# Kernel tuning notes

Hardware: AMD Instinct MI355X
Metric: run time of the kernel (lower is better)

## Reference

```python
import jax, jax.numpy as jnp
import numpy as np

BS, CH, H, W = 4, 64, 32, 88
N_Z = 60
BEV_Z, BEV_X, BEV_Y = 10, 128, 128  # from round((ranges[i+3]-ranges[i])/voxel_size[i])


def setup_inputs() -> dict:
    key = jax.random.key(0)
    k1, k2, k3, k4 = jax.random.split(key, 4)
    x = jax.random.normal(k1, (BS, CH, H, W), dtype=jnp.float32)
    shp = (BS, N_Z, H, W)
    # integer voxel coords, slightly out of range so the kept-mask drops some points
    xi = jax.random.randint(k2, shp, -2, BEV_X + 2)
    yi = jax.random.randint(k3, shp, -2, BEV_Y + 2)
    zi = jax.random.randint(k4, shp, -1, BEV_Z + 1)
    frustum_xyz = jnp.stack([xi, yi, zi], axis=-1).astype(jnp.int32)  # [B,n_z,H,W,3]
    return {"x": x, "frustum_xyz": frustum_xyz}


def reference(x, frustum_xyz):
    # x: [bs, ch, h, w] camera features; frustum_xyz: [bs, n_z, h, w, 3] voxel coords (x, y, z)
    bs, ch, h, w = x.shape
    nz = frustum_xyz.shape[1]
    # permute(0,2,3,1).unsqueeze(1).expand(bs, nz, h, w, ch)
    feats = jnp.broadcast_to(x.transpose(0, 2, 3, 1)[:, None], (bs, nz, h, w, ch)).reshape(-1, ch)
    f = frustum_xyz.reshape(-1, 3)
    xx, yy, zz = f[:, 0], f[:, 1], f[:, 2]
    b = jnp.repeat(jnp.arange(bs, dtype=f.dtype), nz * h * w)  # batch_idx blocks
    kept = ((xx >= 0) & (xx < BEV_X) & (yy >= 0) & (yy < BEV_Y)
            & (zz >= 0) & (zz < BEV_Z))
    # linear voxel index into dense [bs, Z, X, Y]; invalid points go to a dummy segment.
    # sort + cumsum-trick + unique-scatter in the original == per-voxel segment sum.
    nvox = bs * BEV_Z * BEV_X * BEV_Y
    vox = ((b * BEV_Z + zz) * BEV_X + xx) * BEV_Y + yy
    vox = jnp.where(kept, vox, nvox)
    grid = jax.ops.segment_sum(feats, vox, num_segments=nvox + 1)[:-1]  # drop dummy
    grid = grid.reshape(bs, BEV_Z, BEV_X, BEV_Y, ch)
    # final[b, :, z, x, y] = pooled feats; then .sum(-1) over y -> [bs, ch, Z, X]
    return grid.sum(axis=3).transpose(0, 3, 1, 2)
```

## Files before the change

kernel.cpp:

```cpp
#include <hip/hip_runtime.h>
#include <hip/hip_bf16.h>

#define BS    4
#define CH    64
#define HH    32
#define WW    88
#define NZ    60
#define BEV_Z 10
#define BEV_X 128
#define BEV_Y 128

static constexpr int HW        = HH * WW;
static constexpr int ZX        = BEV_Z * BEV_X;
static constexpr int PTS_PER_B = NZ * HW;

static constexpr int T            = 16;
static constexpr int NT           = HW / T;
static constexpr int CNT_BLOCKS   = BS * NT;
static constexpr int NXELEM       = BS * CH * HW;
static constexpr int XCONV_BLOCKS = NXELEM / 4096;
static constexpr int CNT_WORDS    = ZX * T / 4;
static constexpr int TILE_BYTES   = ZX * T;
static constexpr int ZGROUPS      = ZX / 64;

static constexpr int KS     = 22;
static constexpr int KCH    = HW / KS;
static constexpr int OUTSZ  = BS * CH * ZX;

static constexpr int BPTS   = NZ * T;
static constexpr int FSLAB4 = BPTS * 3 / 4;

typedef __attribute__((ext_vector_type(8))) short short8;
typedef __attribute__((ext_vector_type(4))) float floatx4;

__device__ inline unsigned short f2b(float v) {
    __hip_bfloat16 h = __float2bfloat16(v);
    return *reinterpret_cast<unsigned short*>(&h);
}

__device__ inline short cnt2bf(unsigned int w, int s) {
    float fv = (float)((w >> s) & 255u);
    unsigned int u;
    __builtin_memcpy(&u, &fv, 4);
    return (short)(u >> 16);
}

__device__ inline float bfbits2f(unsigned int bits) {
    float fv;
    __builtin_memcpy(&fv, &bits, 4);
    return fv;
}

__global__ __launch_bounds__(256)
void build_kernel(const float* __restrict__ x, const int* __restrict__ f,
                  unsigned int* __restrict__ cnt8,
                  unsigned short* __restrict__ xbf) {
    __shared__ unsigned int cnt[CNT_WORDS];
    __shared__ uint4 fslab[FSLAB4];
    int blk = blockIdx.x;
    if (blk < CNT_BLOCKS) {
        int b   = blk / NT;
        int t   = blk % NT;
        int hw0 = t * T;
        for (int i = threadIdx.x; i < CNT_WORDS; i += 256) cnt[i] = 0u;

        int p0 = b * PTS_PER_B + hw0;
        const uint4* fb = (const uint4*)(f + (size_t)p0 * 3);
        constexpr int SEG4 = HW * 3 / 4;
        for (int i = threadIdx.x; i < FSLAB4; i += 256) {
            int z = i / 12, w16 = i % 12;
            fslab[i] = fb[(size_t)z * SEG4 + w16];
        }
        __syncthreads();

        const unsigned int* fs = (const unsigned int*)fslab;
        #pragma unroll
        for (int r = 0; r < 4; ++r) {
            int j = r * 256 + threadIdx.x;
            if (j < BPTS) {
                int xx = (int)fs[j * 3 + 0];
                int yy = (int)fs[j * 3 + 1];
                int zz = (int)fs[j * 3 + 2];
                bool kept = (xx >= 0) & (xx < BEV_X) & (yy >= 0) & (yy < BEV_Y) &
                            (zz >= 0) & (zz < BEV_Z);
                if (kept) {
                    int hw_l = j & 15;
                    int cell = (zz * BEV_X + xx) * T + hw_l;
                    atomicAdd(&cnt[cell >> 2], 1u << (8 * (cell & 3)));
                }
            }
        }
        __syncthreads();

        unsigned int* obase = cnt8 + (size_t)(b * NT + t) * CNT_WORDS;
        for (int i = threadIdx.x; i < CNT_WORDS; i += 256) obase[i] = cnt[i];
    } else {
        size_t base = (size_t)(blk - CNT_BLOCKS) * 4096;
        #pragma unroll
        for (int r = 0; r < 4; ++r) {
            size_t i = base + ((size_t)r * 256 + threadIdx.x) * 4;
            floatx4 v = *(const floatx4*)(x + i);
            ushort4 o;
            o.x = f2b(v.x); o.y = f2b(v.y); o.z = f2b(v.z); o.w = f2b(v.w);
            *(ushort4*)(xbf + i) = o;
        }
    }
}

__global__ __launch_bounds__(256)
void gemm_kernel(const unsigned short* __restrict__ xbf,
                 const unsigned char* __restrict__ cnt8,
                 unsigned short* __restrict__ P) {
    int blk  = blockIdx.x;
    int kc   = blk % KS;
    int r2   = blk / KS;
    int b    = r2 / ZGROUPS;
    int zg   = r2 % ZGROUPS;
    int wave = threadIdx.x >> 6;
    int lane = threadIdx.x & 63;
    int m    = lane & 15;
    int quad = lane >> 4;
    int zx   = zg * 64 + wave * 16 + m;
    int k0   = kc * KCH;

    const unsigned char* pb = cnt8 + (size_t)b * NT * TILE_BYTES
                            + (size_t)(k0 / T + (quad >> 1)) * TILE_BYTES
                            + zx * T + (quad & 1) * 8;
    const unsigned short* pa = xbf + ((size_t)(b * CH) + m) * HW + k0 + quad * 8;

    uint2 wv[4];
    short8 a[4][4];
    #pragma unroll
    for (int i = 0; i < 4; ++i) {
        wv[i] = *(const uint2*)(pb + (size_t)(2 * i) * TILE_BYTES);
        #pragma unroll
        for (int c = 0; c < 4; ++c)
            a[i][c] = *(const short8*)(pa + c * 16 * HW + i * 32);
    }

    floatx4 acc0 = {0.f,0.f,0.f,0.f}, acc1 = {0.f,0.f,0.f,0.f};
    floatx4 acc2 = {0.f,0.f,0.f,0.f}, acc3 = {0.f,0.f,0.f,0.f};

    #pragma unroll
    for (int i = 0; i < 4; ++i) {
        short8 bf;
        bf[0] = cnt2bf(wv[i].x,  0); bf[1] = cnt2bf(wv[i].x,  8);
        bf[2] = cnt2bf(wv[i].x, 16); bf[3] = cnt2bf(wv[i].x, 24);
        bf[4] = cnt2bf(wv[i].y,  0); bf[5] = cnt2bf(wv[i].y,  8);
        bf[6] = cnt2bf(wv[i].y, 16); bf[7] = cnt2bf(wv[i].y, 24);
        acc0 = __builtin_amdgcn_mfma_f32_16x16x32_bf16(a[i][0], bf, acc0, 0, 0, 0);
        acc1 = __builtin_amdgcn_mfma_f32_16x16x32_bf16(a[i][1], bf, acc1, 0, 0, 0);
        acc2 = __builtin_amdgcn_mfma_f32_16x16x32_bf16(a[i][2], bf, acc2, 0, 0, 0);
        acc3 = __builtin_amdgcn_mfma_f32_16x16x32_bf16(a[i][3], bf, acc3, 0, 0, 0);
    }

    unsigned short* op = P + ((size_t)(kc * BS + b) * CH) * ZX + zx;
    #pragma unroll
    for (int r = 0; r < 4; ++r) {
        int ch = quad * 4 + r;
        op[(0 * 16 + ch) * ZX] = f2b(acc0[r]);
        op[(1 * 16 + ch) * ZX] = f2b(acc1[r]);
        op[(2 * 16 + ch) * ZX] = f2b(acc2[r]);
        op[(3 * 16 + ch) * ZX] = f2b(acc3[r]);
    }
}

__global__ __launch_bounds__(256)
void reduce_kernel(const unsigned int* __restrict__ P, float* __restrict__ out) {
    int idx = blockIdx.x * 256 + threadIdx.x;
    float s_lo = 0.f, s_hi = 0.f;
    #pragma unroll
    for (int kc = 0; kc < KS; ++kc) {
        unsigned int u = P[(size_t)kc * (OUTSZ / 2) + idx];
        s_lo += bfbits2f(u << 16);
        s_hi += bfbits2f(u & 0xFFFF0000u);
    }
    *(float2*)(out + (size_t)idx * 2) = make_float2(s_lo, s_hi);
}

extern "C" void kernel_launch(void* const* d_in, const int* in_sizes, int n_in,
                              void* d_out, int out_size, void* d_ws, size_t ws_size,
                              hipStream_t stream) {
    const float* x = (const float*)d_in[0];
    const int*   f = (const int*)d_in[1];
    float*       out = (float*)d_out;

    char* ws = (char*)d_ws;
    size_t off = 0;
    auto carve = [&](size_t bytes) {
        char* p = ws + off;
        off += (bytes + 255) & ~(size_t)255;
        return p;
    };
    unsigned int*   cnt8 = (unsigned int*)  carve((size_t)BS * NT * TILE_BYTES);
    unsigned short* xbf  = (unsigned short*)carve((size_t)NXELEM * 2);
    unsigned short* P    = (unsigned short*)carve((size_t)KS * OUTSZ * 2);

    build_kernel <<<CNT_BLOCKS + XCONV_BLOCKS, 256, 0, stream>>>(x, f, cnt8, xbf);
    gemm_kernel  <<<BS * ZGROUPS * KS, 256, 0, stream>>>(xbf, (const unsigned char*)cnt8, P);
    reduce_kernel<<<OUTSZ / 2 / 256, 256, 0, stream>>>((const unsigned int*)P, out);
}
```

Baseline: 90.23 us.

## Fuse split-K GEMM and reduction into one kernel with in-block LDS reduction

Replaces the 22-way split-K GEMM, which wrote bf16 partials to a workspace for a separate reduce kernel, with one 1024-thread block per 16-column zx tile. Each block's 16 waves cover 4 channel groups by 4 K-quarters, loop over K with a 4-deep register prefetch, and reduce the K-quarters through shared memory before writing fp32 output directly. This removes one kernel launch, the partial-sum global traffic and the bf16 rounding of partials. In exchange each wave runs a much longer serial MFMA chain on a single accumulator, and the grid is 320 blocks of 1024 threads.

Result: no change. 91.85 us (+1.8%).

```diff
diff --git a/kernel.cpp b/kernel.cpp
--- a/kernel.cpp
+++ b/kernel.cpp
@@ -21,14 +21,13 @@
 static constexpr int XCONV_BLOCKS = NXELEM / 4096;
 static constexpr int CNT_WORDS    = ZX * T / 4;
 static constexpr int TILE_BYTES   = ZX * T;
-static constexpr int ZGROUPS      = ZX / 64;
-
-static constexpr int KS     = 22;
-static constexpr int KCH    = HW / KS;
-static constexpr int OUTSZ  = BS * CH * ZX;
 
 static constexpr int BPTS   = NZ * T;
 static constexpr int FSLAB4 = BPTS * 3 / 4;
+
+static constexpr int NZG    = ZX / 16;
+static constexpr int QK     = HW / 4;
+static constexpr int ITERS  = QK / 32;
 
 typedef __attribute__((ext_vector_type(8))) short short8;
 typedef __attribute__((ext_vector_type(4))) float floatx4;
@@ -43,12 +42,6 @@
     unsigned int u;
     __builtin_memcpy(&u, &fv, 4);
     return (short)(u >> 16);
-}
-
-__device__ inline float bfbits2f(unsigned int bits) {
-    float fv;
-    __builtin_memcpy(&fv, &bits, 4);
-    return fv;
 }
 
 __global__ __launch_bounds__(256)
@@ -107,75 +100,65 @@
     }
 }
 
-__global__ __launch_bounds__(256)
-void gemm_kernel(const unsigned short* __restrict__ xbf,
-                 const unsigned char* __restrict__ cnt8,
-                 unsigned short* __restrict__ P) {
+__global__ __launch_bounds__(1024, 8)
+void gemm_fused(const unsigned short* __restrict__ xbf,
+                const unsigned char* __restrict__ cnt8,
+                float* __restrict__ out) {
+    __shared__ floatx4 red[3][4][64];
     int blk  = blockIdx.x;
-    int kc   = blk % KS;
-    int r2   = blk / KS;
-    int b    = r2 / ZGROUPS;
-    int zg   = r2 % ZGROUPS;
-    int wave = threadIdx.x >> 6;
+    int b    = blk / NZG;
+    int zx0  = (blk % NZG) * 16;
+    int wid  = threadIdx.x >> 6;
+    int c    = wid & 3;
+    int q    = wid >> 2;
     int lane = threadIdx.x & 63;
     int m    = lane & 15;
     int quad = lane >> 4;
-    int zx   = zg * 64 + wave * 16 + m;
-    int k0   = kc * KCH;
+    int zx   = zx0 + m;
 
     const unsigned char* pb = cnt8 + (size_t)b * NT * TILE_BYTES
-                            + (size_t)(k0 / T + (quad >> 1)) * TILE_BYTES
+                            + (size_t)(q * (QK / T) + (quad >> 1)) * TILE_BYTES
                             + zx * T + (quad & 1) * 8;
-    const unsigned short* pa = xbf + ((size_t)(b * CH) + m) * HW + k0 + quad * 8;
+    const unsigned short* pa = xbf + ((size_t)(b * CH) + c * 16 + m) * HW
+                             + q * QK + quad * 8;
 
-    uint2 wv[4];
-    short8 a[4][4];
+    uint2  wv[4];
+    short8 av[4];
     #pragma unroll
     for (int i = 0; i < 4; ++i) {
         wv[i] = *(const uint2*)(pb + (size_t)(2 * i) * TILE_BYTES);
-        #pragma unroll
-        for (int c = 0; c < 4; ++c)
-            a[i][c] = *(const short8*)(pa + c * 16 * HW + i * 32);
+        av[i] = *(const short8*)(pa + i * 32);
     }
 
-    floatx4 acc0 = {0.f,0.f,0.f,0.f}, acc1 = {0.f,0.f,0.f,0.f};
-    floatx4 acc2 = {0.f,0.f,0.f,0.f}, acc3 = {0.f,0.f,0.f,0.f};
-
+    floatx4 acc = {0.f, 0.f, 0.f, 0.f};
     #pragma unroll
-    for (int i = 0; i < 4; ++i) {
+    for (int i = 0; i < ITERS; ++i) {
+        int s = i & 3;
+        uint2  w = wv[s];
+        short8 a = av[s];
+        if (i + 4 < ITERS) {
+            wv[s] = *(const uint2*)(pb + (size_t)(2 * (i + 4)) * TILE_BYTES);
+            av[s] = *(const short8*)(pa + (i + 4) * 32);
+        }
         short8 bf;
-        bf[0] = cnt2bf(wv[i].x,  0); bf[1] = cnt2bf(wv[i].x,  8);
-        bf[2] = cnt2bf(wv[i].x, 16); bf[3] = cnt2bf(wv[i].x, 24);
-        bf[4] = cnt2bf(wv[i].y,  0); bf[5] = cnt2bf(wv[i].y,  8);
-        bf[6] = cnt2bf(wv[i].y, 16); bf[7] = cnt2bf(wv[i].y, 24);
-        acc0 = __builtin_amdgcn_mfma_f32_16x16x32_bf16(a[i][0], bf, acc0, 0, 0, 0);
-        acc1 = __builtin_amdgcn_mfma_f32_16x16x32_bf16(a[i][1], bf, acc1, 0, 0, 0);
-        acc2 = __builtin_amdgcn_mfma_f32_16x16x32_bf16(a[i][2], bf, acc2, 0, 0, 0);
-        acc3 = __builtin_amdgcn_mfma_f32_16x16x32_bf16(a[i][3], bf, acc3, 0, 0, 0);
+        bf[0] = cnt2bf(w.x,  0); bf[1] = cnt2bf(w.x,  8);
+        bf[2] = cnt2bf(w.x, 16); bf[3] = cnt2bf(w.x, 24);
+        bf[4] = cnt2bf(w.y,  0); bf[5] = cnt2bf(w.y,  8);
+        bf[6] = cnt2bf(w.y, 16); bf[7] = cnt2bf(w.y, 24);
+        acc = __builtin_amdgcn_mfma_f32_16x16x32_bf16(a, bf, acc, 0, 0, 0);
     }
 
-    unsigned short* op = P + ((size_t)(kc * BS + b) * CH) * ZX + zx;
-    #pragma unroll
-    for (int r = 0; r < 4; ++r) {
-        int ch = quad * 4 + r;
-        op[(0 * 16 + ch) * ZX] = f2b(acc0[r]);
-        op[(1 * 16 + ch) * ZX] = f2b(acc1[r]);
-        op[(2 * 16 + ch) * ZX] = f2b(acc2[r]);
-        op[(3 * 16 + ch) * ZX] = f2b(acc3[r]);
+    if (q) red[q - 1][c][lane] = acc;
+    __syncthreads();
+    if (q == 0) {
+        floatx4 r0 = red[0][c][lane];
+        floatx4 r1 = red[1][c][lane];
+        floatx4 r2 = red[2][c][lane];
+        acc += r0 + r1 + r2;
+        float* ob = out + ((size_t)(b * CH + c * 16 + quad * 4)) * ZX + zx;
+        #pragma unroll
+        for (int r = 0; r < 4; ++r) ob[r * ZX] = acc[r];
     }
-}
-
-__global__ __launch_bounds__(256)
-void reduce_kernel(const unsigned int* __restrict__ P, float* __restrict__ out) {
-    int idx = blockIdx.x * 256 + threadIdx.x;
-    float s_lo = 0.f, s_hi = 0.f;
-    #pragma unroll
-    for (int kc = 0; kc < KS; ++kc) {
-        unsigned int u = P[(size_t)kc * (OUTSZ / 2) + idx];
-        s_lo += bfbits2f(u << 16);
-        s_hi += bfbits2f(u & 0xFFFF0000u);
-    }
-    *(float2*)(out + (size_t)idx * 2) = make_float2(s_lo, s_hi);
 }
 
 extern "C" void kernel_launch(void* const* d_in, const int* in_sizes, int n_in,
@@ -194,9 +177,7 @@
     };
     unsigned int*   cnt8 = (unsigned int*)  carve((size_t)BS * NT * TILE_BYTES);
     unsigned short* xbf  = (unsigned short*)carve((size_t)NXELEM * 2);
-    unsigned short* P    = (unsigned short*)carve((size_t)KS * OUTSZ * 2);
 
-    build_kernel <<<CNT_BLOCKS + XCONV_BLOCKS, 256, 0, stream>>>(x, f, cnt8, xbf);
-    gemm_kernel  <<<BS * ZGROUPS * KS, 256, 0, stream>>>(xbf, (const unsigned char*)cnt8, P);
-    reduce_kernel<<<OUTSZ / 2 / 256, 256, 0, stream>>>((const unsigned int*)P, out);
+    build_kernel<<<CNT_BLOCKS + XCONV_BLOCKS, 256, 0, stream>>>(x, f, cnt8, xbf);
+    gemm_fused  <<<BS * NZG, 1024, 0, stream>>>(xbf, (const unsigned char*)cnt8, out);
 }
```

## Halve GEMM K-splits and double-buffer operand loads per block

Applied to the files above, without the earlier changes.

Halves the number of K-split partial slices (22 to 11), so each GEMM block processes 256 instead of 128 K elements. It uses a rolling register prefetch: the second half's operands load while the first half's MFMAs run. This cuts the partial-sum buffer and the reduce kernel's reads in half, at the cost of fewer, longer GEMM blocks and more register pressure (capped via launch bounds). The kept-mask check is also simplified to unsigned comparisons.

New measurement: 89.40 us. About the same (-0.9%).

```diff
diff --git a/kernel.cpp b/kernel.cpp
--- a/kernel.cpp
+++ b/kernel.cpp
@@ -23,7 +23,7 @@
 static constexpr int TILE_BYTES   = ZX * T;
 static constexpr int ZGROUPS      = ZX / 64;
 
-static constexpr int KS     = 22;
+static constexpr int KS     = 11;
 static constexpr int KCH    = HW / KS;
 static constexpr int OUTSZ  = BS * CH * ZX;
 
@@ -81,8 +81,8 @@
                 int xx = (int)fs[j * 3 + 0];
                 int yy = (int)fs[j * 3 + 1];
                 int zz = (int)fs[j * 3 + 2];
-                bool kept = (xx >= 0) & (xx < BEV_X) & (yy >= 0) & (yy < BEV_Y) &
-                            (zz >= 0) & (zz < BEV_Z);
+                bool kept = ((unsigned)xx < BEV_X) & ((unsigned)yy < BEV_Y) &
+                            ((unsigned)zz < BEV_Z);
                 if (kept) {
                     int hw_l = j & 15;
                     int cell = (zz * BEV_X + xx) * T + hw_l;
@@ -107,7 +107,7 @@
     }
 }
 
-__global__ __launch_bounds__(256)
+__global__ __launch_bounds__(256, 4)
 void gemm_kernel(const unsigned short* __restrict__ xbf,
                  const unsigned char* __restrict__ cnt8,
                  unsigned short* __restrict__ P) {
@@ -128,30 +128,40 @@
                             + zx * T + (quad & 1) * 8;
     const unsigned short* pa = xbf + ((size_t)(b * CH) + m) * HW + k0 + quad * 8;
 
-    uint2 wv[4];
-    short8 a[4][4];
+    uint2  wv[4];
+    short8 av[4][4];
     #pragma unroll
     for (int i = 0; i < 4; ++i) {
         wv[i] = *(const uint2*)(pb + (size_t)(2 * i) * TILE_BYTES);
         #pragma unroll
         for (int c = 0; c < 4; ++c)
-            a[i][c] = *(const short8*)(pa + c * 16 * HW + i * 32);
+            av[i][c] = *(const short8*)(pa + c * 16 * HW + i * 32);
     }
 
     floatx4 acc0 = {0.f,0.f,0.f,0.f}, acc1 = {0.f,0.f,0.f,0.f};
     floatx4 acc2 = {0.f,0.f,0.f,0.f}, acc3 = {0.f,0.f,0.f,0.f};
 
     #pragma unroll
-    for (int i = 0; i < 4; ++i) {
+    for (int i = 0; i < 8; ++i) {
+        int s = i & 3;
+        uint2  w  = wv[s];
+        short8 a0 = av[s][0], a1 = av[s][1], a2 = av[s][2], a3 = av[s][3];
+        if (i < 4) {
+            wv[s] = *(const uint2*)(pb + (size_t)(2 * (i + 4)) * TILE_BYTES);
+            #pragma unroll
+            for (int c = 0; c < 4; ++c)
+                av[s][c] = *(const short8*)(pa + c * 16 * HW + (i + 4) * 32);
+        }
         short8 bf;
-        bf[0] = cnt2bf(wv[i].x,  0); bf[1] = cnt2bf(wv[i].x,  8);
-        bf[2] = cnt2bf(wv[i].x, 16); bf[3] = cnt2bf(wv[i].x, 24);
-        bf[4] = cnt2bf(wv[i].y,  0); bf[5] = cnt2bf(wv[i].y,  8);
-        bf[6] = cnt2bf(wv[i].y, 16); bf[7] = cnt2bf(wv[i].y, 24);
-        acc0 = __builtin_amdgcn_mfma_f32_16x16x32_bf16(a[i][0], bf, acc0, 0, 0, 0);
-        acc1 = __builtin_amdgcn_mfma_f32_16x16x32_bf16(a[i][1], bf, acc1, 0, 0, 0);
-        acc2 = __builtin_amdgcn_mfma_f32_16x16x32_bf16(a[i][2], bf, acc2, 0, 0, 0);
-        acc3 = __builtin_amdgcn_mfma_f32_16x16x32_bf16(a[i][3], bf, acc3, 0, 0, 0);
+        bf[0] = cnt2bf(w.x,  0); bf[1] = cnt2bf(w.x,  8);
+        bf[2] = cnt2bf(w.x, 16); bf[3] = cnt2bf(w.x, 24);
+        bf[4] = cnt2bf(w.y,  0); bf[5] = cnt2bf(w.y,  8);
+        bf[6] = cnt2bf(w.y, 16); bf[7] = cnt2bf(w.y, 24);
+
+        acc0 = __builtin_amdgcn_mfma_f32_16x16x32_bf16(a0, bf, acc0, 0, 0, 0);
+        acc1 = __builtin_amdgcn_mfma_f32_16x16x32_bf16(a1, bf, acc1, 0, 0, 0);
+        acc2 = __builtin_amdgcn_mfma_f32_16x16x32_bf16(a2, bf, acc2, 0, 0, 0);
+        acc3 = __builtin_amdgcn_mfma_f32_16x16x32_bf16(a3, bf, acc3, 0, 0, 0);
     }
 
     unsigned short* op = P + ((size_t)(kc * BS + b) * CH) * ZX + zx;
```
